# Kernel tuning notes

Measured on AMD Instinct MI355X. Metric: run time of the kernel, lower is better.

Reference implementation:

```python
import jax, jax.numpy as jnp
import numpy as np

B, N, C = 4, 2048, 64   # batch, tokens, num_feat
HS = 512                # hidden_size
H = HS // C             # 8 heads, head_dim = C = 64
EPS = 1e-6


def _ln(x, g, b):
    m = x.mean(-1, keepdims=True)
    v = ((x - m) ** 2).mean(-1, keepdims=True)
    return (x - m) / jnp.sqrt(v + EPS) * g + b


def setup_inputs() -> dict:
    key = jax.random.key(0)
    ks = jax.random.split(key, 8)
    s = 0.02
    return {
        "x": jax.random.normal(ks[0], (B, N, C), jnp.float32),
        "g1": jnp.ones((C,), jnp.float32),
        "be1": jnp.zeros((C,), jnp.float32),
        "Wqkv": jax.random.normal(ks[1], (C, 3 * HS), jnp.float32) * s,
        "bqkv": jnp.zeros((3 * HS,), jnp.float32),
        "Wout": jax.random.normal(ks[2], (HS, C), jnp.float32) * s,
        "bout": jnp.zeros((C,), jnp.float32),
        "g2": jnp.ones((C,), jnp.float32),
        "be2": jnp.zeros((C,), jnp.float32),
        "W1": jax.random.normal(ks[3], (C, HS // 8), jnp.float32) * s,
        "b1": jax.random.normal(ks[4], (HS // 8,), jnp.float32) * 1e-6,
        "W2": jax.random.normal(ks[5], (HS // 8, C), jnp.float32) * s,
        "b2": jax.random.normal(ks[6], (C,), jnp.float32) * 1e-6,
    }


def reference(x, g1, be1, Wqkv, bqkv, Wout, bout, g2, be2, W1, b1, W2, b2):
    b_, n_, c_ = x.shape
    hs = Wout.shape[0]
    h_ = hs // c_
    res = x
    y = _ln(x, g1, be1)
    # fused QKV: (B,N,3*HS) -> (3,B,H,N,D) with D = c_
    qkv = (y @ Wqkv + bqkv).reshape(b_, n_, 3, h_, c_).transpose(2, 0, 3, 1, 4)
    q, k, v = qkv[0], qkv[1], qkv[2]
    scores = jnp.einsum('bhqd,bhkd->bhqk', q, k) / jnp.sqrt(jnp.asarray(c_, x.dtype))
    probs = jax.nn.softmax(scores, axis=-1)
    ctx = jnp.einsum('bhqk,bhkd->bhqd', probs, v)
    ctx = ctx.transpose(0, 2, 1, 3).reshape(b_, n_, hs)
    attn = jax.nn.gelu(ctx @ Wout + bout, approximate=False)  # GELU after out proj per source
    x2 = attn + res
    y2 = _ln(x2, g2, be2)
    mlp = jax.nn.gelu(y2 @ W1 + b1, approximate=False) @ W2 + b2
    return mlp + x2
```

## Files before the change

### kernel.cpp

```cpp
#include <hip/hip_runtime.h>


#define NN 2048
#define CC 64
#define HH 8
#define HSZ 512

typedef __bf16 bf16x8 __attribute__((ext_vector_type(8)));
typedef float f32x4 __attribute__((ext_vector_type(4)));

__device__ __forceinline__ float b2f(unsigned short u) {
  union { unsigned int i; float f; } v; v.i = ((unsigned int)u) << 16; return v.f;
}
__device__ __forceinline__ unsigned short f2b(float f) {
  union { float f; unsigned int i; } v; v.f = f;
  unsigned int r = v.i + 0x7FFFu + ((v.i >> 16) & 1u);
  return (unsigned short)(r >> 16);
}
__device__ __forceinline__ unsigned int pk2(float a, float b) {
  return (unsigned int)f2b(a) | ((unsigned int)f2b(b) << 16);
}
__device__ __forceinline__ float gelu_f(float x) {
  return 0.5f * x * (1.0f + erff(x * 0.7071067811865475f));
}

__global__ __launch_bounds__(256) void k_ln_qkv(
    const float* __restrict__ x,
    const float* __restrict__ g1,
    const float* __restrict__ be1,
    const float* __restrict__ W,
    const float* __restrict__ bqkv,
    unsigned short* __restrict__ Qb,
    unsigned short* __restrict__ Kb,
    unsigned short* __restrict__ Vb)
{
  __shared__ __align__(16) unsigned short As[64 * 72];
  __shared__ __align__(16) unsigned short Ws[128 * 72];
  const int tid = threadIdx.x, wv = tid >> 6, lane = tid & 63;
  const int col = lane & 15, quad = lane >> 4;
  const int bm = blockIdx.x & 127, bn = blockIdx.x >> 7;
  const int m0 = bm * 64, nw = bn * 128;

  const int c4 = tid & 15;
  float4 gv = *(const float4*)(g1 + c4 * 4);
  float4 bv = *(const float4*)(be1 + c4 * 4);
  #pragma unroll
  for (int s = 0; s < 4; ++s) {
    int idx = s * 256 + tid;
    int row = idx >> 4;
    float4 xv = *(const float4*)(x + (size_t)(m0 + row) * CC + c4 * 4);
    float ps = xv.x + xv.y + xv.z + xv.w;
    float ps2 = xv.x * xv.x + xv.y * xv.y + xv.z * xv.z + xv.w * xv.w;
    #pragma unroll
    for (int off = 8; off; off >>= 1) {
      ps += __shfl_xor(ps, off, 16);
      ps2 += __shfl_xor(ps2, off, 16);
    }
    float mean = ps * (1.0f / 64.0f);
    float var = ps2 * (1.0f / 64.0f) - mean * mean;
    float rs = rsqrtf(var + 1e-6f);
    uint2 packed;
    packed.x = pk2((xv.x - mean) * rs * gv.x + bv.x, (xv.y - mean) * rs * gv.y + bv.y);
    packed.y = pk2((xv.z - mean) * rs * gv.z + bv.z, (xv.w - mean) * rs * gv.w + bv.w);
    *(uint2*)&As[row * 72 + c4 * 4] = packed;
  }

  {
    const int c_loc = tid & 127;
    const int kg = tid >> 7;
    const int ng = nw + c_loc;
    #pragma unroll
    for (int g = 0; g < 4; ++g) {
      float wv8[8];
      #pragma unroll
      for (int j = 0; j < 8; ++j) wv8[j] = W[(size_t)(kg * 32 + g * 8 + j) * 1536 + ng];
      uint4 u;
      u.x = pk2(wv8[0], wv8[1]); u.y = pk2(wv8[2], wv8[3]);
      u.z = pk2(wv8[4], wv8[5]); u.w = pk2(wv8[6], wv8[7]);
      *(uint4*)&Ws[c_loc * 72 + kg * 32 + g * 8] = u;
    }
  }
  __syncthreads();

  bf16x8 af0 = *(const bf16x8*)&As[(wv * 16 + col) * 72 + quad * 8];
  bf16x8 af1 = *(const bf16x8*)&As[(wv * 16 + col) * 72 + 32 + quad * 8];

  f32x4 acc[8];
  #pragma unroll
  for (int nt = 0; nt < 8; ++nt) acc[nt] = (f32x4){0.f, 0.f, 0.f, 0.f};
  #pragma unroll
  for (int nt = 0; nt < 8; ++nt) {
    bf16x8 b0 = *(const bf16x8*)&Ws[(nt * 16 + col) * 72 + quad * 8];
    bf16x8 b1 = *(const bf16x8*)&Ws[(nt * 16 + col) * 72 + 32 + quad * 8];
    acc[nt] = __builtin_amdgcn_mfma_f32_16x16x32_bf16(af0, b0, acc[nt], 0, 0, 0);
    acc[nt] = __builtin_amdgcn_mfma_f32_16x16x32_bf16(af1, b1, acc[nt], 0, 0, 0);
  }

  #pragma unroll
  for (int nt = 0; nt < 8; ++nt) {
    const int n0 = nw + nt * 16;
    const int which = n0 >> 9;
    const int h = (n0 >> 6) & 7;
    const int d0 = n0 & 63;
    unsigned short* dst = (which == 0) ? Qb : (which == 1) ? Kb : Vb;
    const float scale = (which == 0) ? 0.125f : 1.0f;
    const float bias = bqkv[n0 + col];
    #pragma unroll
    for (int r = 0; r < 4; ++r) {
      int tk = m0 + wv * 16 + quad * 4 + r;
      int bb = tk >> 11, nn = tk & 2047;
      dst[((size_t)(bb * HH + h) * NN + nn) * CC + d0 + col] =
          f2b((acc[nt][r] + bias) * scale);
    }
  }
}

__global__ __launch_bounds__(256) void k_vt(
    const unsigned short* __restrict__ Vb,
    unsigned short* __restrict__ VbT)
{
  __shared__ __align__(16) unsigned short Ld[128 * 72];
  const int tid = threadIdx.x, lane = tid & 63;
  const int bh = blockIdx.x >> 4, tc = blockIdx.x & 15;
  const size_t base = (size_t)bh * NN * CC;
  const int t0 = tc * 128;

  #pragma unroll
  for (int p = 0; p < 4; ++p) {
    int idx = p * 256 + tid;
    int row = idx >> 3, c8 = (idx & 7) << 3;
    *(uint4*)&Ld[row * 72 + c8] = *(const uint4*)(Vb + base + (size_t)(t0 + row) * CC + c8);
  }
  __syncthreads();

  const int tl = (tid & 15) * 8;
  const int rot = lane & 7;
  #pragma unroll
  for (int p = 0; p < 4; ++p) {
    int d = p * 16 + (tid >> 4);
    alignas(16) unsigned short tm[8];
    #pragma unroll
    for (int j = 0; j < 8; ++j) {
      int jj = (j + rot) & 7;
      tm[jj] = Ld[(tl + jj) * 72 + d];
    }
    *(uint4*)(VbT + base + (size_t)d * NN + t0 + tl) = *(const uint4*)tm;
  }
}

__global__ __launch_bounds__(256) void k_attn(
    const unsigned short* __restrict__ Q,
    const unsigned short* __restrict__ K,
    const unsigned short* __restrict__ VT,
    const float* __restrict__ Wout,
    unsigned short* __restrict__ part)
{
  __shared__ __align__(16) unsigned short Ks[64 * 72];
  __shared__ __align__(16) unsigned short Vt[64 * 72];
  __shared__ __align__(16) unsigned short Ps[4][16 * 72];
  const int tid = threadIdx.x, wv = tid >> 6, lane = tid & 63;
  const int col = lane & 15, quad = lane >> 4;
  const int bh = blockIdx.x >> 5, qc = blockIdx.x & 31;
  const size_t base = (size_t)bh * NN * CC;
  const int q0 = qc * 64 + wv * 16;

  bf16x8 qf0 = *(const bf16x8*)(Q + base + (size_t)(q0 + col) * CC + quad * 8);
  bf16x8 qf1 = *(const bf16x8*)(Q + base + (size_t)(q0 + col) * CC + 32 + quad * 8);

  f32x4 o[4];
  float lsum[4] = {0.f, 0.f, 0.f, 0.f};
  #pragma unroll
  for (int dt = 0; dt < 4; ++dt) o[dt] = (f32x4){0.f, 0.f, 0.f, 0.f};
  unsigned short* Pw = Ps[wv];

  for (int kt = 0; kt < 32; ++kt) {
    const int kb = kt * 64;
    #pragma unroll
    for (int p = 0; p < 2; ++p) {
      int idx = p * 256 + tid;
      int r = idx >> 3, c8 = (idx & 7) << 3;
      *(uint4*)&Ks[r * 72 + c8] = *(const uint4*)(K + base + (size_t)(kb + r) * CC + c8);
      *(uint4*)&Vt[r * 72 + c8] = *(const uint4*)(VT + base + (size_t)r * NN + kb + c8);
    }
    __syncthreads();

    #pragma unroll
    for (int ct = 0; ct < 4; ++ct) {
      bf16x8 k0 = *(const bf16x8*)&Ks[(ct * 16 + col) * 72 + quad * 8];
      bf16x8 k1 = *(const bf16x8*)&Ks[(ct * 16 + col) * 72 + 32 + quad * 8];
      f32x4 a = (f32x4){0.f, 0.f, 0.f, 0.f};
      a = __builtin_amdgcn_mfma_f32_16x16x32_bf16(qf0, k0, a, 0, 0, 0);
      a = __builtin_amdgcn_mfma_f32_16x16x32_bf16(qf1, k1, a, 0, 0, 0);
      #pragma unroll
      for (int r = 0; r < 4; ++r) {
        float pv = __expf(a[r]);
        lsum[r] += pv;
        Pw[(quad * 4 + r) * 72 + ct * 16 + col] = f2b(pv);
      }
    }
    bf16x8 pa0 = *(const bf16x8*)&Pw[col * 72 + quad * 8];
    bf16x8 pa1 = *(const bf16x8*)&Pw[col * 72 + 32 + quad * 8];
    #pragma unroll
    for (int dt = 0; dt < 4; ++dt) {
      bf16x8 v0 = *(const bf16x8*)&Vt[(dt * 16 + col) * 72 + quad * 8];
      bf16x8 v1 = *(const bf16x8*)&Vt[(dt * 16 + col) * 72 + 32 + quad * 8];
      o[dt] = __builtin_amdgcn_mfma_f32_16x16x32_bf16(pa0, v0, o[dt], 0, 0, 0);
      o[dt] = __builtin_amdgcn_mfma_f32_16x16x32_bf16(pa1, v1, o[dt], 0, 0, 0);
    }
    __syncthreads();
  }

  #pragma unroll
  for (int r = 0; r < 4; ++r) {
    float v = lsum[r];
    #pragma unroll
    for (int off = 8; off; off >>= 1) v += __shfl_xor(v, off, 16);
    float inv = 1.0f / v;
    #pragma unroll
    for (int dt = 0; dt < 4; ++dt) o[dt][r] *= inv;
  }

  const int h = bh & 7, b = bh >> 3;
  {
    const int c = tid & 63, kg = tid >> 6;
    #pragma unroll
    for (int j = 0; j < 16; ++j) {
      float wval = Wout[(size_t)(h * 64 + kg * 16 + j) * 64 + c];
      Ks[c * 72 + kg * 16 + j] = f2b(wval);
    }
  }
  #pragma unroll
  for (int dt = 0; dt < 4; ++dt)
    #pragma unroll
    for (int r = 0; r < 4; ++r)
      Pw[(quad * 4 + r) * 72 + dt * 16 + col] = f2b(o[dt][r]);
  __syncthreads();

  bf16x8 oa0 = *(const bf16x8*)&Pw[col * 72 + quad * 8];
  bf16x8 oa1 = *(const bf16x8*)&Pw[col * 72 + 32 + quad * 8];
  #pragma unroll
  for (int nt = 0; nt < 4; ++nt) {
    bf16x8 bw0 = *(const bf16x8*)&Ks[(nt * 16 + col) * 72 + quad * 8];
    bf16x8 bw1 = *(const bf16x8*)&Ks[(nt * 16 + col) * 72 + 32 + quad * 8];
    f32x4 ac = (f32x4){0.f, 0.f, 0.f, 0.f};
    ac = __builtin_amdgcn_mfma_f32_16x16x32_bf16(oa0, bw0, ac, 0, 0, 0);
    ac = __builtin_amdgcn_mfma_f32_16x16x32_bf16(oa1, bw1, ac, 0, 0, 0);
    #pragma unroll
    for (int r = 0; r < 4; ++r) {
      int n = q0 + quad * 4 + r;
      part[((size_t)(b * HH + h) * NN + n) * CC + nt * 16 + col] = f2b(ac[r]);
    }
  }
}

__global__ __launch_bounds__(256) void k_post(
    const unsigned short* __restrict__ part,
    const float* __restrict__ x,
    const float* __restrict__ bout,
    const float* __restrict__ g2,
    const float* __restrict__ be2,
    const float* __restrict__ W1,
    const float* __restrict__ b1,
    const float* __restrict__ W2,
    const float* __restrict__ b2v,
    float* __restrict__ out)
{
  __shared__ __align__(16) float Ws1[64 * 64];
  __shared__ __align__(16) float Ws2[64 * 64];
  __shared__ float ys[4][64], hs[4][64];
  const int tid = threadIdx.x, wid = tid >> 6, lane = tid & 63;
  const int tk = blockIdx.x * 4 + wid;
  const int b = tk >> 11, n = tk & 2047;

  #pragma unroll
  for (int p = 0; p < 4; ++p) {
    int idx = p * 256 + tid;
    *(float4*)&Ws1[idx * 4] = *(const float4*)(W1 + idx * 4);
    *(float4*)&Ws2[idx * 4] = *(const float4*)(W2 + idx * 4);
  }

  float proj = 0.f;
  #pragma unroll
  for (int h = 0; h < 8; ++h)
    proj += b2f(part[((size_t)(b * HH + h) * NN + n) * CC + lane]);

  float a = gelu_f(proj + bout[lane]);
  float x2 = a + x[(size_t)tk * CC + lane];
  float s = x2;
  #pragma unroll
  for (int off = 32; off; off >>= 1) s += __shfl_xor(s, off, 64);
  float mean = s * (1.0f / 64.0f);
  float d = x2 - mean;
  float vs = d * d;
  #pragma unroll
  for (int off = 32; off; off >>= 1) vs += __shfl_xor(vs, off, 64);
  float var = vs * (1.0f / 64.0f);
  ys[wid][lane] = d * rsqrtf(var + 1e-6f) * g2[lane] + be2[lane];
  __syncthreads();

  float acc2 = 0.f;
  #pragma unroll 8
  for (int c = 0; c < 64; ++c) acc2 += ys[wid][c] * Ws1[c * 64 + lane];
  hs[wid][lane] = gelu_f(acc2 + b1[lane]);

  float acc3 = 0.f;
  #pragma unroll 8
  for (int c = 0; c < 64; ++c) acc3 += hs[wid][c] * Ws2[c * 64 + lane];
  out[(size_t)tk * CC + lane] = acc3 + b2v[lane] + x2;
}

extern "C" void kernel_launch(void* const* d_in, const int* in_sizes, int n_in,
                              void* d_out, int out_size, void* d_ws, size_t ws_size,
                              hipStream_t stream) {
  const float* x    = (const float*)d_in[0];
  const float* g1   = (const float*)d_in[1];
  const float* be1  = (const float*)d_in[2];
  const float* Wqkv = (const float*)d_in[3];
  const float* bqkv = (const float*)d_in[4];
  const float* Wout = (const float*)d_in[5];
  const float* bout = (const float*)d_in[6];
  const float* g2   = (const float*)d_in[7];
  const float* be2  = (const float*)d_in[8];
  const float* W1   = (const float*)d_in[9];
  const float* b1   = (const float*)d_in[10];
  const float* W2   = (const float*)d_in[11];
  const float* b2   = (const float*)d_in[12];
  float* out = (float*)d_out;

  unsigned short* ws = (unsigned short*)d_ws;
  const size_t SZ = (size_t)4 * HH * NN * CC;
  unsigned short* Qb  = ws;
  unsigned short* Kb  = ws + SZ;
  unsigned short* Vb  = ws + 2 * SZ;
  unsigned short* VbT = ws + 3 * SZ;

  k_ln_qkv<<<1536, 256, 0, stream>>>(x, g1, be1, Wqkv, bqkv, Qb, Kb, Vb);
  k_vt<<<512, 256, 0, stream>>>(Vb, VbT);
  k_attn<<<1024, 256, 0, stream>>>(Qb, Kb, VbT, Wout, Qb);
  k_post<<<2048, 256, 0, stream>>>(Qb, x, bout, g2, be2, W1, b1, W2, b2, out);
}
```

Before: 183.0 us.

## Store Q/K/V in FP8, use FP8 MFMA in attention, write V transposed directly

Result: faster. 170.0 us (-7.1%).

```diff
diff --git a/kernel.cpp b/kernel.cpp
--- a/kernel.cpp
+++ b/kernel.cpp
@@ -19,6 +19,10 @@
 }
 __device__ __forceinline__ unsigned int pk2(float a, float b) {
   return (unsigned int)f2b(a) | ((unsigned int)f2b(b) << 16);
+}
+__device__ __forceinline__ unsigned char f2fp8(float f) {
+  int p = __builtin_amdgcn_cvt_pk_fp8_f32(f, f, 0, false);
+  return (unsigned char)(p & 0xFF);
 }
 __device__ __forceinline__ float gelu_f(float x) {
   return 0.5f * x * (1.0f + erff(x * 0.7071067811865475f));
@@ -30,9 +34,9 @@
     const float* __restrict__ be1,
     const float* __restrict__ W,
     const float* __restrict__ bqkv,
-    unsigned short* __restrict__ Qb,
-    unsigned short* __restrict__ Kb,
-    unsigned short* __restrict__ Vb)
+    unsigned char* __restrict__ Qb,
+    unsigned char* __restrict__ Kb,
+    unsigned char* __restrict__ VbT)
 {
   __shared__ __align__(16) unsigned short As[64 * 72];
   __shared__ __align__(16) unsigned short Ws[128 * 72];
@@ -96,116 +100,92 @@
     acc[nt] = __builtin_amdgcn_mfma_f32_16x16x32_bf16(af1, b1, acc[nt], 0, 0, 0);
   }
 
+  const int tkb = m0 + wv * 16 + quad * 4;
+  const int bb = tkb >> 11;
+  const int nnb = tkb & 2047;
   #pragma unroll
   for (int nt = 0; nt < 8; ++nt) {
     const int n0 = nw + nt * 16;
     const int which = n0 >> 9;
     const int h = (n0 >> 6) & 7;
     const int d0 = n0 & 63;
-    unsigned short* dst = (which == 0) ? Qb : (which == 1) ? Kb : Vb;
-    const float scale = (which == 0) ? 0.125f : 1.0f;
     const float bias = bqkv[n0 + col];
-    #pragma unroll
-    for (int r = 0; r < 4; ++r) {
-      int tk = m0 + wv * 16 + quad * 4 + r;
-      int bb = tk >> 11, nn = tk & 2047;
-      dst[((size_t)(bb * HH + h) * NN + nn) * CC + d0 + col] =
-          f2b((acc[nt][r] + bias) * scale);
-    }
-  }
-}
-
-__global__ __launch_bounds__(256) void k_vt(
-    const unsigned short* __restrict__ Vb,
-    unsigned short* __restrict__ VbT)
-{
-  __shared__ __align__(16) unsigned short Ld[128 * 72];
-  const int tid = threadIdx.x, lane = tid & 63;
-  const int bh = blockIdx.x >> 4, tc = blockIdx.x & 15;
-  const size_t base = (size_t)bh * NN * CC;
-  const int t0 = tc * 128;
-
-  #pragma unroll
-  for (int p = 0; p < 4; ++p) {
-    int idx = p * 256 + tid;
-    int row = idx >> 3, c8 = (idx & 7) << 3;
-    *(uint4*)&Ld[row * 72 + c8] = *(const uint4*)(Vb + base + (size_t)(t0 + row) * CC + c8);
-  }
-  __syncthreads();
-
-  const int tl = (tid & 15) * 8;
-  const int rot = lane & 7;
-  #pragma unroll
-  for (int p = 0; p < 4; ++p) {
-    int d = p * 16 + (tid >> 4);
-    alignas(16) unsigned short tm[8];
-    #pragma unroll
-    for (int j = 0; j < 8; ++j) {
-      int jj = (j + rot) & 7;
-      tm[jj] = Ld[(tl + jj) * 72 + d];
-    }
-    *(uint4*)(VbT + base + (size_t)d * NN + t0 + tl) = *(const uint4*)tm;
+    float vv[4];
+    #pragma unroll
+    for (int r = 0; r < 4; ++r) vv[r] = acc[nt][r] + bias;
+    if (which == 2) {
+      int lo = __builtin_amdgcn_cvt_pk_fp8_f32(vv[0], vv[1], 0, false);
+      int full = __builtin_amdgcn_cvt_pk_fp8_f32(vv[2], vv[3], lo, true);
+      *(unsigned int*)(VbT + ((size_t)(bb * HH + h) * CC + d0 + col) * NN + nnb) =
+          (unsigned int)full;
+    } else {
+      unsigned char* dst = (which == 0) ? Qb : Kb;
+      #pragma unroll
+      for (int r = 0; r < 4; ++r)
+        dst[((size_t)(bb * HH + h) * NN + nnb + r) * CC + d0 + col] = f2fp8(vv[r]);
+    }
   }
 }
 
 __global__ __launch_bounds__(256) void k_attn(
-    const unsigned short* __restrict__ Q,
-    const unsigned short* __restrict__ K,
-    const unsigned short* __restrict__ VT,
+    const unsigned char* __restrict__ Q,
+    const unsigned char* __restrict__ K,
+    const unsigned char* __restrict__ VT,
     const float* __restrict__ Wout,
     unsigned short* __restrict__ part)
 {
-  __shared__ __align__(16) unsigned short Ks[64 * 72];
-  __shared__ __align__(16) unsigned short Vt[64 * 72];
-  __shared__ __align__(16) unsigned short Ps[4][16 * 72];
+  __shared__ __align__(16) unsigned char smem[18432];
+  unsigned char* Ks = smem;
+  unsigned char* Vt = smem + 5120;
+  unsigned char* Ps = smem + 10240;
+  unsigned short* Wb = (unsigned short*)smem;
+  unsigned short* Ob = (unsigned short*)(smem + 9216);
   const int tid = threadIdx.x, wv = tid >> 6, lane = tid & 63;
   const int col = lane & 15, quad = lane >> 4;
   const int bh = blockIdx.x >> 5, qc = blockIdx.x & 31;
   const size_t base = (size_t)bh * NN * CC;
   const int q0 = qc * 64 + wv * 16;
 
-  bf16x8 qf0 = *(const bf16x8*)(Q + base + (size_t)(q0 + col) * CC + quad * 8);
-  bf16x8 qf1 = *(const bf16x8*)(Q + base + (size_t)(q0 + col) * CC + 32 + quad * 8);
+  long qf0 = *(const long*)(Q + base + (size_t)(q0 + col) * CC + quad * 8);
+  long qf1 = *(const long*)(Q + base + (size_t)(q0 + col) * CC + 32 + quad * 8);
 
   f32x4 o[4];
   float lsum[4] = {0.f, 0.f, 0.f, 0.f};
   #pragma unroll
   for (int dt = 0; dt < 4; ++dt) o[dt] = (f32x4){0.f, 0.f, 0.f, 0.f};
-  unsigned short* Pw = Ps[wv];
+  unsigned char* Pw = Ps + wv * (16 * 80);
 
   for (int kt = 0; kt < 32; ++kt) {
     const int kb = kt * 64;
-    #pragma unroll
-    for (int p = 0; p < 2; ++p) {
-      int idx = p * 256 + tid;
-      int r = idx >> 3, c8 = (idx & 7) << 3;
-      *(uint4*)&Ks[r * 72 + c8] = *(const uint4*)(K + base + (size_t)(kb + r) * CC + c8);
-      *(uint4*)&Vt[r * 72 + c8] = *(const uint4*)(VT + base + (size_t)r * NN + kb + c8);
+    {
+      int row = tid >> 2, c16 = (tid & 3) << 4;
+      *(uint4*)&Ks[row * 80 + c16] = *(const uint4*)(K + base + (size_t)(kb + row) * CC + c16);
+      *(uint4*)&Vt[row * 80 + c16] = *(const uint4*)(VT + base + (size_t)row * NN + kb + c16);
     }
     __syncthreads();
 
     #pragma unroll
     for (int ct = 0; ct < 4; ++ct) {
-      bf16x8 k0 = *(const bf16x8*)&Ks[(ct * 16 + col) * 72 + quad * 8];
-      bf16x8 k1 = *(const bf16x8*)&Ks[(ct * 16 + col) * 72 + 32 + quad * 8];
+      long k0 = *(const long*)&Ks[(ct * 16 + col) * 80 + quad * 8];
+      long k1 = *(const long*)&Ks[(ct * 16 + col) * 80 + 32 + quad * 8];
       f32x4 a = (f32x4){0.f, 0.f, 0.f, 0.f};
-      a = __builtin_amdgcn_mfma_f32_16x16x32_bf16(qf0, k0, a, 0, 0, 0);
-      a = __builtin_amdgcn_mfma_f32_16x16x32_bf16(qf1, k1, a, 0, 0, 0);
+      a = __builtin_amdgcn_mfma_f32_16x16x32_fp8_fp8(qf0, k0, a, 0, 0, 0);
+      a = __builtin_amdgcn_mfma_f32_16x16x32_fp8_fp8(qf1, k1, a, 0, 0, 0);
       #pragma unroll
       for (int r = 0; r < 4; ++r) {
-        float pv = __expf(a[r]);
+        float pv = __expf(a[r] * 0.125f);
         lsum[r] += pv;
-        Pw[(quad * 4 + r) * 72 + ct * 16 + col] = f2b(pv);
+        Pw[(quad * 4 + r) * 80 + ct * 16 + col] = f2fp8(pv);
       }
     }
-    bf16x8 pa0 = *(const bf16x8*)&Pw[col * 72 + quad * 8];
-    bf16x8 pa1 = *(const bf16x8*)&Pw[col * 72 + 32 + quad * 8];
+    long pa0 = *(const long*)&Pw[col * 80 + quad * 8];
+    long pa1 = *(const long*)&Pw[col * 80 + 32 + quad * 8];
     #pragma unroll
     for (int dt = 0; dt < 4; ++dt) {
-      bf16x8 v0 = *(const bf16x8*)&Vt[(dt * 16 + col) * 72 + quad * 8];
-      bf16x8 v1 = *(const bf16x8*)&Vt[(dt * 16 + col) * 72 + 32 + quad * 8];
-      o[dt] = __builtin_amdgcn_mfma_f32_16x16x32_bf16(pa0, v0, o[dt], 0, 0, 0);
-      o[dt] = __builtin_amdgcn_mfma_f32_16x16x32_bf16(pa1, v1, o[dt], 0, 0, 0);
+      long v0 = *(const long*)&Vt[(dt * 16 + col) * 80 + quad * 8];
+      long v1 = *(const long*)&Vt[(dt * 16 + col) * 80 + 32 + quad * 8];
+      o[dt] = __builtin_amdgcn_mfma_f32_16x16x32_fp8_fp8(pa0, v0, o[dt], 0, 0, 0);
+      o[dt] = __builtin_amdgcn_mfma_f32_16x16x32_fp8_fp8(pa1, v1, o[dt], 0, 0, 0);
     }
     __syncthreads();
   }
@@ -224,24 +204,23 @@
   {
     const int c = tid & 63, kg = tid >> 6;
     #pragma unroll
-    for (int j = 0; j < 16; ++j) {
-      float wval = Wout[(size_t)(h * 64 + kg * 16 + j) * 64 + c];
-      Ks[c * 72 + kg * 16 + j] = f2b(wval);
-    }
-  }
+    for (int j = 0; j < 16; ++j)
+      Wb[c * 72 + kg * 16 + j] = f2b(Wout[(size_t)(h * 64 + kg * 16 + j) * 64 + c]);
+  }
+  unsigned short* Obw = Ob + wv * (16 * 72);
   #pragma unroll
   for (int dt = 0; dt < 4; ++dt)
     #pragma unroll
     for (int r = 0; r < 4; ++r)
-      Pw[(quad * 4 + r) * 72 + dt * 16 + col] = f2b(o[dt][r]);
+      Obw[(quad * 4 + r) * 72 + dt * 16 + col] = f2b(o[dt][r]);
   __syncthreads();
 
-  bf16x8 oa0 = *(const bf16x8*)&Pw[col * 72 + quad * 8];
-  bf16x8 oa1 = *(const bf16x8*)&Pw[col * 72 + 32 + quad * 8];
+  bf16x8 oa0 = *(const bf16x8*)&Obw[col * 72 + quad * 8];
+  bf16x8 oa1 = *(const bf16x8*)&Obw[col * 72 + 32 + quad * 8];
   #pragma unroll
   for (int nt = 0; nt < 4; ++nt) {
-    bf16x8 bw0 = *(const bf16x8*)&Ks[(nt * 16 + col) * 72 + quad * 8];
-    bf16x8 bw1 = *(const bf16x8*)&Ks[(nt * 16 + col) * 72 + 32 + quad * 8];
+    bf16x8 bw0 = *(const bf16x8*)&Wb[(nt * 16 + col) * 72 + quad * 8];
+    bf16x8 bw1 = *(const bf16x8*)&Wb[(nt * 16 + col) * 72 + 32 + quad * 8];
     f32x4 ac = (f32x4){0.f, 0.f, 0.f, 0.f};
     ac = __builtin_amdgcn_mfma_f32_16x16x32_bf16(oa0, bw0, ac, 0, 0, 0);
     ac = __builtin_amdgcn_mfma_f32_16x16x32_bf16(oa1, bw1, ac, 0, 0, 0);
@@ -327,15 +306,14 @@
   const float* b2   = (const float*)d_in[12];
   float* out = (float*)d_out;
 
-  unsigned short* ws = (unsigned short*)d_ws;
+  unsigned char* wsb = (unsigned char*)d_ws;
   const size_t SZ = (size_t)4 * HH * NN * CC;
-  unsigned short* Qb  = ws;
-  unsigned short* Kb  = ws + SZ;
-  unsigned short* Vb  = ws + 2 * SZ;
-  unsigned short* VbT = ws + 3 * SZ;
-
-  k_ln_qkv<<<1536, 256, 0, stream>>>(x, g1, be1, Wqkv, bqkv, Qb, Kb, Vb);
-  k_vt<<<512, 256, 0, stream>>>(Vb, VbT);
-  k_attn<<<1024, 256, 0, stream>>>(Qb, Kb, VbT, Wout, Qb);
-  k_post<<<2048, 256, 0, stream>>>(Qb, x, bout, g2, be2, W1, b1, W2, b2, out);
-}
+  unsigned char* Qb   = wsb;
+  unsigned char* Kb   = wsb + SZ;
+  unsigned char* VbT  = wsb + 2 * SZ;
+  unsigned short* part = (unsigned short*)(wsb + 3 * SZ);
+
+  k_ln_qkv<<<1536, 256, 0, stream>>>(x, g1, be1, Wqkv, bqkv, Qb, Kb, VbT);
+  k_attn<<<1024, 256, 0, stream>>>(Qb, Kb, VbT, Wout, part);
+  k_post<<<2048, 256, 0, stream>>>(part, x, bout, g2, be2, W1, b1, W2, b2, out);
+}
```
